# Performance work log

Measured on AMD Instinct MI355X. Metric: run time of the kernel, lower is better.

Reference implementation:

```python
import jax, jax.numpy as jnp
import numpy as np


def _rank_transform_ascending(flat):
    # torch: _, idx = sort(flat, descending=False); flat[idx] = linspace(0,1,n)+1/n
    n = flat.shape[0]
    order = jnp.argsort(flat)  # ascending
    prob = jnp.linspace(0.0, 1.0, n, dtype=flat.dtype) + jnp.asarray(1.0 / n, flat.dtype)
    return jnp.zeros_like(flat).at[order].set(prob)


def corr_attention(query, key, value):
    # score[b,h,i,j] = cosine-like similarity q_i . k_j / (|q_i| |k_j|)
    score = jnp.einsum('bhid,bhjd->bhij', query, key)
    q_len = jnp.sqrt(jnp.sum(query * query, axis=-1, keepdims=True)) + 1e-5  # [b,h,s,1]
    k_len = jnp.sqrt(jnp.sum(key * key, axis=-1, keepdims=True)) + 1e-5      # [b,h,s,1]
    score = score / (q_len * jnp.swapaxes(k_len, -1, -2))
    signal = jnp.sign(score)
    size = score.shape
    flat = jnp.abs(score).reshape(-1)
    ranked = _rank_transform_ascending(flat)
    score = -jnp.log(ranked).reshape(size) * signal
    score = score / jnp.sum(jnp.abs(score), axis=-1, keepdims=True)
    return jnp.einsum('bhij,bhjd->bhid', score, value)


def setup_inputs() -> dict:
    key0 = jax.random.key(0)
    kq, kk, kv = jax.random.split(key0, 3)
    B, H, S, D = 4, 8, 1024, 64
    query = jax.random.normal(kq, (B, H, S, D), dtype=jnp.float32)
    key = jax.random.normal(kk, (B, H, S, D), dtype=jnp.float32)
    value = jax.random.normal(kv, (B, H, S, D), dtype=jnp.float32)
    return {"query": query, "key": key, "value": value}


def reference(query, key, value):
    # Attention.forward with mode='season'
    return corr_attention(query, key, value)
```

## Files before the change

kernel.cpp:

```cpp
#include <hip/hip_runtime.h>
#include <math.h>
#include <stdint.h>

#define S_LEN 1024
#define D_DIM 64
#define BH    32
#define KSHIFT 13
#define NBINS 130048u
#define PV_LO  119808u
#define NPVT   10240u
#define HIST_LO 117760u
#define NHOT_H  12288u
#define NCHUNK 254
#define HBLK   256
#define INV_NM1 (1.0f/33554431.0f)
#define INV_N   (2.9802322387695312e-08f)
#define FIX_TH  1e-4f


typedef _Float16 half8 __attribute__((ext_vector_type(8)));
typedef short    short8 __attribute__((ext_vector_type(8)));
typedef float    floatx4 __attribute__((ext_vector_type(4)));

__global__ __launch_bounds__(256) void norms_kernel(
    const float* __restrict__ Q, const float* __restrict__ K,
    double* __restrict__ qinvD, double* __restrict__ kinvD,
    float* __restrict__ qinvF, float* __restrict__ kinvF) {
  int row  = blockIdx.x * 4 + (threadIdx.x >> 6);
  int lane = threadIdx.x & 63;
  const float* src; double* dstD; float* dstF; int r = row;
  if (row < BH * S_LEN) { src = Q; dstD = qinvD; dstF = qinvF; }
  else                  { src = K; dstD = kinvD; dstF = kinvF; r = row - BH * S_LEN; }
  double v = (double)src[(size_t)r * D_DIM + lane];
  double s = v * v;
  #pragma unroll
  for (int off = 32; off; off >>= 1) s += __shfl_down(s, off);
  if (lane == 0) {
    double inv = 1.0 / (sqrt(s) + 1e-5);
    dstD[r] = inv;
    dstF[r] = (float)inv;
  }
}

__device__ __forceinline__ void bf16_split(float x, short& hi, short& lo) {
  unsigned u = __float_as_uint(x);
  unsigned h = (u + 0x7FFFu + ((u >> 16) & 1u)) >> 16;
  float hf = __uint_as_float(h << 16);
  float lf = x - hf;
  hi = (short)h;
  lo = (short)(__float_as_uint(lf) >> 16);
}

__global__ __launch_bounds__(256) void qk_mfma_kernel(
    const float* __restrict__ Q, const float* __restrict__ K,
    const float* __restrict__ qinvF, const float* __restrict__ kinvF,
    float* __restrict__ score) {
  __shared__ short Qhi[64][72], Qlo[64][72];
  __shared__ short Khi[64][72], Klo[64][72];
  int bh = blockIdx.z;
  int i0 = blockIdx.y * 64;
  int j0 = blockIdx.x * 64;
  int tid = threadIdx.x;
  const float* Qb = Q + ((size_t)bh * S_LEN + i0) * D_DIM;
  const float* Kb = K + ((size_t)bh * S_LEN + j0) * D_DIM;
  #pragma unroll
  for (int l = 0; l < 4; ++l) {
    int idx4 = l * 256 + tid;
    int row  = idx4 >> 4;
    int c4   = idx4 & 15;
    float qi = qinvF[(size_t)bh * S_LEN + i0 + row];
    float4 v = ((const float4*)Qb)[idx4];
    float qv[4] = {v.x * qi, v.y * qi, v.z * qi, v.w * qi};
    short qh[4], ql[4];
    #pragma unroll
    for (int c = 0; c < 4; ++c) bf16_split(qv[c], qh[c], ql[c]);
    *(short4*)&Qhi[row][c4 * 4] = make_short4(qh[0], qh[1], qh[2], qh[3]);
    *(short4*)&Qlo[row][c4 * 4] = make_short4(ql[0], ql[1], ql[2], ql[3]);
    float kj = kinvF[(size_t)bh * S_LEN + j0 + row];
    float4 w = ((const float4*)Kb)[idx4];
    float kv[4] = {w.x * kj, w.y * kj, w.z * kj, w.w * kj};
    short kh[4], kl[4];
    #pragma unroll
    for (int c = 0; c < 4; ++c) bf16_split(kv[c], kh[c], kl[c]);
    *(short4*)&Khi[row][c4 * 4] = make_short4(kh[0], kh[1], kh[2], kh[3]);
    *(short4*)&Klo[row][c4 * 4] = make_short4(kl[0], kl[1], kl[2], kl[3]);
  }
  __syncthreads();
  int wave = tid >> 6;
  int lane = tid & 63;
  int m    = lane & 15;
  int quad = lane >> 4;
  floatx4 acc[4];
  #pragma unroll
  for (int n = 0; n < 4; ++n) acc[n] = (floatx4){0.f, 0.f, 0.f, 0.f};
  #pragma unroll
  for (int ks = 0; ks < 2; ++ks) {
    int kb = ks * 32 + quad * 8;
    short8 a_hi = *(const short8*)&Qhi[wave * 16 + m][kb];
    short8 a_lo = *(const short8*)&Qlo[wave * 16 + m][kb];
    #pragma unroll
    for (int nt = 0; nt < 4; ++nt) {
      short8 b_hi = *(const short8*)&Khi[nt * 16 + m][kb];
      short8 b_lo = *(const short8*)&Klo[nt * 16 + m][kb];
      acc[nt] = __builtin_amdgcn_mfma_f32_16x16x32_bf16(a_hi, b_hi, acc[nt], 0, 0, 0);
      acc[nt] = __builtin_amdgcn_mfma_f32_16x16x32_bf16(a_hi, b_lo, acc[nt], 0, 0, 0);
      acc[nt] = __builtin_amdgcn_mfma_f32_16x16x32_bf16(a_lo, b_hi, acc[nt], 0, 0, 0);
    }
  }
  #pragma unroll
  for (int r = 0; r < 4; ++r) {
    float* op = score + (size_t)bh * 1048576 + (size_t)(j0 >> 6) * 65536
              + (size_t)(i0 + wave * 16 + quad * 4 + r) * 64 + m;
    #pragma unroll
    for (int nt = 0; nt < 4; ++nt)
      op[nt * 16] = acc[nt][r];
  }
}

__global__ __launch_bounds__(1024) void hist_kernel(
    float* __restrict__ score, const float* __restrict__ Q, const float* __restrict__ K,
    const double* __restrict__ qinvD, const double* __restrict__ kinvD,
    unsigned* __restrict__ hist, unsigned char* __restrict__ partial) {
  __shared__ unsigned lh[NHOT_H];
  int tid = threadIdx.x;
  int lane = tid & 63;
  for (unsigned i = tid; i < NHOT_H; i += 1024) lh[i] = 0u;
  __syncthreads();
  const float4* p = (const float4*)score + (size_t)blockIdx.x * 32768;
  #pragma unroll 2
  for (int it = 0; it < 32; ++it) {
    float4 v = p[it * 1024 + tid];
    float vv[4] = {v.x, v.y, v.z, v.w};
    bool anyf = (fabsf(vv[0]) < FIX_TH) | (fabsf(vv[1]) < FIX_TH) |
                (fabsf(vv[2]) < FIX_TH) | (fabsf(vv[3]) < FIX_TH);
    unsigned long long am = __ballot(anyf);
    while (am) {
      int src = (int)(__ffsll((long long)am) - 1);
      am &= am - 1;
      unsigned base4 = (unsigned)(blockIdx.x * 32768u + (unsigned)(it * 1024 + tid));
      unsigned b4 = __shfl(base4, src);
      #pragma unroll
      for (int c = 0; c < 4; ++c) {
        float sc = __shfl(vv[c], src);
        if (fabsf(sc) < FIX_TH) {
          unsigned flat = b4 * 4u + (unsigned)c;
          unsigned bh = flat >> 20;
          unsigned rem = flat & 0xFFFFFu;
          unsigned jt = rem >> 16;
          unsigned i  = (rem >> 6) & 1023u;
          unsigned j  = jt * 64u + (rem & 63u);
          double qd = (double)Q[((size_t)bh * S_LEN + i) * D_DIM + lane];
          double kd = (double)K[((size_t)bh * S_LEN + j) * D_DIM + lane];
          double pd = qd * kd;
          #pragma unroll
          for (int off = 32; off; off >>= 1) pd += __shfl_down(pd, off);
          float corr = 0.f;
          if (lane == 0)
            corr = (float)(pd * qinvD[(size_t)bh * S_LEN + i] * kinvD[(size_t)bh * S_LEN + j]);
          corr = __shfl(corr, 0);
          if (lane == src) {
            vv[c] = corr;
            score[(size_t)flat] = corr;
          }
        }
      }
    }
    #pragma unroll
    for (int c = 0; c < 4; ++c) {
      unsigned b = __float_as_uint(fabsf(vv[c])) >> KSHIFT;
      if (b >= NBINS) b = NBINS - 1u;
      if (b >= HIST_LO) atomicAdd(&lh[b - HIST_LO], 1u);
      else              atomicAdd(&hist[b], 1u);
    }
  }
  __syncthreads();
  unsigned char* dst = partial + (size_t)blockIdx.x * NHOT_H;
  for (unsigned i = tid; i < NHOT_H; i += 1024) dst[i] = (unsigned char)lh[i];
}

__global__ __launch_bounds__(256) void hreduce_kernel(
    const unsigned char* __restrict__ partial, unsigned* __restrict__ hist) {
  unsigned bin = blockIdx.x * 256 + threadIdx.x;
  unsigned s = 0;
  #pragma unroll 8
  for (int b = 0; b < HBLK; ++b) s += (unsigned)partial[(size_t)b * NHOT_H + bin];
  hist[HIST_LO + bin] = s;
}

__global__ __launch_bounds__(256) void vt_kernel(
    const float* __restrict__ V, _Float16* __restrict__ Vt) {
  __shared__ _Float16 T[64][72];
  int bh = blockIdx.y, j0 = blockIdx.x * 64, tid = threadIdx.x;
  const float* Vb = V + ((size_t)bh * S_LEN + j0) * D_DIM;
  #pragma unroll
  for (int l = 0; l < 4; ++l) {
    int idx = l * 256 + tid;
    int jr = idx >> 4, d4 = idx & 15;
    float4 v = ((const float4*)Vb)[idx];
    T[d4*4+0][jr] = (_Float16)v.x;
    T[d4*4+1][jr] = (_Float16)v.y;
    T[d4*4+2][jr] = (_Float16)v.z;
    T[d4*4+3][jr] = (_Float16)v.w;
  }
  __syncthreads();
  _Float16* Ob = Vt + (size_t)(bh * 16 + blockIdx.x) * 4096;
  #pragma unroll
  for (int l = 0; l < 2; ++l) {
    int idx = l * 256 + tid;
    int d = idx >> 3, jc = idx & 7;
    uint4 val = *(const uint4*)&T[d][jc*8];
    *(uint4*)(Ob + (size_t)d * 64 + jc*8) = val;
  }
}

__global__ __launch_bounds__(256) void scan1_kernel(const unsigned* __restrict__ hist,
                                                    unsigned* __restrict__ csum) {
  __shared__ unsigned sd[256];
  int c = blockIdx.x, t = threadIdx.x;
  const unsigned* p = hist + (size_t)c * 512;
  sd[t] = p[t] + p[t + 256];
  __syncthreads();
  for (int off = 128; off; off >>= 1) {
    if (t < off) sd[t] += sd[t + off];
    __syncthreads();
  }
  if (t == 0) csum[c] = sd[0];
}

__global__ __launch_bounds__(256) void scan2_kernel(unsigned* __restrict__ csum) {
  __shared__ unsigned d[256];
  int t = threadIdx.x;
  unsigned v = (t < NCHUNK) ? csum[t] : 0u;
  d[t] = v; __syncthreads();
  for (int off = 1; off < 256; off <<= 1) {
    unsigned x = (t >= off) ? d[t - off] : 0u;
    __syncthreads();
    d[t] += x;
    __syncthreads();
  }
  if (t < NCHUNK) csum[t] = d[t] - v;
}

__global__ __launch_bounds__(256) void scan3_kernel(const unsigned* __restrict__ hist,
                                                    const unsigned* __restrict__ csum,
                                                    _Float16* __restrict__ tTab16) {
  __shared__ unsigned ts[256];
  int c = blockIdx.x, t = threadIdx.x;
  const unsigned* p = hist + (size_t)c * 512 + t * 2;
  unsigned l0 = p[0], l1 = p[1];
  unsigned s = l0 + l1;
  ts[t] = s; __syncthreads();
  for (int off = 1; off < 256; off <<= 1) {
    unsigned x = (t >= off) ? ts[t - off] : 0u;
    __syncthreads();
    ts[t] += x;
    __syncthreads();
  }
  unsigned base = csum[c] + ts[t] - s;
  int idx = c * 512 + t * 2;
  float r0 = (float)base + 0.5f * ((float)l0 - 1.0f);
  tTab16[idx]     = (_Float16)(-__logf(fmaf(r0, INV_NM1, INV_N)));
  float r1 = (float)(base + l0) + 0.5f * ((float)l1 - 1.0f);
  tTab16[idx + 1] = (_Float16)(-__logf(fmaf(r1, INV_NM1, INV_N)));
}

__global__ __launch_bounds__(256) void pv_mfma_kernel(
    const float* __restrict__ score, const _Float16* __restrict__ Vt,
    const unsigned short* __restrict__ tTab16, float* __restrict__ out) {
  __shared__ unsigned short ldsT[NPVT];
  __shared__ float red[4352];
  int tid = threadIdx.x;
  {
    const unsigned* gsrc = (const unsigned*)(tTab16 + PV_LO);
    unsigned* ldst = (unsigned*)ldsT;
    #pragma unroll
    for (int i = 0; i < 20; ++i)
      ldst[i * 256 + tid] = gsrc[i * 256 + tid];
  }
  __syncthreads();

  int bh   = blockIdx.y;
  int wave = tid >> 6;
  int lane = tid & 63;
  int m    = lane & 15;
  int quad = lane >> 4;
  int i0   = blockIdx.x * 16;
  const float*    Sb = score + (size_t)bh * 1048576 + (size_t)(i0 + m) * 64;
  const _Float16* Vb = Vt + (size_t)bh * 65536;
  floatx4 acc[4];
  #pragma unroll
  for (int n = 0; n < 4; ++n) acc[n] = (floatx4){0.f, 0.f, 0.f, 0.f};
  float rsum = 0.f;

  for (int ks = 0; ks < 8; ++ks) {
    int k0  = wave * 256 + ks * 32 + quad * 8;
    int jt  = k0 >> 6;
    int jin = k0 & 63;
    const float* sp = Sb + (size_t)jt * 65536 + jin;
    float4 s0 = *(const float4*)(sp);
    float4 s1 = *(const float4*)(sp + 4);
    float sv[8] = {s0.x, s0.y, s0.z, s0.w, s1.x, s1.y, s1.z, s1.w};
    union { unsigned short u[8]; half8 h; } af;
    #pragma unroll
    for (int e = 0; e < 8; ++e) {
      unsigned u = __float_as_uint(sv[e]);
      unsigned a = u & 0x7fffffffu;
      unsigned b = a >> KSHIFT;
      if (b > NBINS - 1u) b = NBINS - 1u;
      unsigned short tb;
      if (b >= PV_LO) tb = ldsT[b - PV_LO];
      else            tb = tTab16[b];
      if (a == 0u) tb = 0;
      af.u[e] = (unsigned short)(tb ^ ((u >> 16) & 0x8000u));
      unsigned short tabs = (unsigned short)(tb & 0x7fffu);
      _Float16 th = __builtin_bit_cast(_Float16, tabs);
      rsum += (float)th;
    }
    half8 bf[4];
    #pragma unroll
    for (int n = 0; n < 4; ++n)
      bf[n] = *(const half8*)(Vb + (size_t)jt * 4096 + (size_t)(n * 16 + m) * 64 + jin);
    #pragma unroll
    for (int n = 0; n < 4; ++n)
      acc[n] = __builtin_amdgcn_mfma_f32_16x16x32_f16(af.h, bf[n], acc[n], 0, 0, 0);
  }

  #pragma unroll
  for (int n = 0; n < 4; ++n)
    #pragma unroll
    for (int r = 0; r < 4; ++r)
      red[(wave * 16 + quad * 4 + r) * 64 + n * 16 + m] = acc[n][r];
  red[4096 + wave * 64 + lane] = rsum;
  __syncthreads();

  int col = tid & 63;
  int rq  = tid >> 6;
  #pragma unroll
  for (int t = 0; t < 4; ++t) {
    int row = rq * 4 + t;
    float s = 0.f;
    #pragma unroll
    for (int w = 0; w < 4; ++w) s += red[(w * 16 + row) * 64 + col];
    float rs = 0.f;
    #pragma unroll
    for (int w = 0; w < 4; ++w)
      #pragma unroll
      for (int q = 0; q < 4; ++q)
        rs += red[4096 + w * 64 + q * 16 + row];
    out[((size_t)bh * S_LEN + i0 + row) * D_DIM + col] = s / rs;
  }
}

extern "C" void kernel_launch(void* const* d_in, const int* in_sizes, int n_in,
                              void* d_out, int out_size, void* d_ws, size_t ws_size,
                              hipStream_t stream) {
  const float* Q = (const float*)d_in[0];
  const float* K = (const float*)d_in[1];
  const float* V = (const float*)d_in[2];
  float* out = (float*)d_out;
  char* ws = (char*)d_ws;
  float*         score   = (float*)(ws);
  unsigned*      hist    = (unsigned*)(ws + 134217728);
  unsigned char* partial = (unsigned char*)(ws + 134737920);
  double*        qinvD   = (double*)(ws + 137883648);
  double*        kinvD   = (double*)(ws + 138145792);
  float*         qinvF   = (float*)(ws + 138407936);
  float*         kinvF   = (float*)(ws + 138539008);
  _Float16*      Vt      = (_Float16*)(ws + 134737920);
  unsigned*      csum    = (unsigned*)(ws + 139194368);
  _Float16*      tTab16  = (_Float16*)(ws + 139195392);

  hipMemsetAsync(hist, 0, NBINS * sizeof(unsigned), stream);
  norms_kernel<<<(2 * BH * S_LEN) / 4, 256, 0, stream>>>(Q, K, qinvD, kinvD, qinvF, kinvF);
  qk_mfma_kernel<<<dim3(16, 16, BH), 256, 0, stream>>>(Q, K, qinvF, kinvF, score);
  hist_kernel<<<HBLK, 1024, 0, stream>>>(score, Q, K, qinvD, kinvD, hist, partial);
  hreduce_kernel<<<NHOT_H / 256, 256, 0, stream>>>(partial, hist);
  vt_kernel<<<dim3(16, BH), 256, 0, stream>>>(V, Vt);
  scan1_kernel<<<NCHUNK, 256, 0, stream>>>(hist, csum);
  scan2_kernel<<<1, 256, 0, stream>>>(csum);
  scan3_kernel<<<NCHUNK, 256, 0, stream>>>(hist, csum, tTab16);
  pv_mfma_kernel<<<dim3(S_LEN / 16, BH), 256, 0, stream>>>(
      score, Vt, (const unsigned short*)tTab16, out);
}
```

Baseline: 217.5 us.

## Store 16-bit bin codes instead of fp32 scores, fuse near-zero fixup into QK

```diff
diff --git a/kernel.cpp b/kernel.cpp
--- a/kernel.cpp
+++ b/kernel.cpp
@@ -7,11 +7,13 @@
 #define BH    32
 #define KSHIFT 13
 #define NBINS 130048u
-#define PV_LO  119808u
+#define CODE_BASE 97280u
+#define NB2   32768u
+#define HIST_LO_C 20480u
+#define NHOT_H  12288u
+#define PV_LO_C 22528u
 #define NPVT   10240u
-#define HIST_LO 117760u
-#define NHOT_H  12288u
-#define NCHUNK 254
+#define NCHUNK 64
 #define HBLK   256
 #define INV_NM1 (1.0f/33554431.0f)
 #define INV_N   (2.9802322387695312e-08f)
@@ -54,7 +56,8 @@
 __global__ __launch_bounds__(256) void qk_mfma_kernel(
     const float* __restrict__ Q, const float* __restrict__ K,
     const float* __restrict__ qinvF, const float* __restrict__ kinvF,
-    float* __restrict__ score) {
+    const double* __restrict__ qinvD, const double* __restrict__ kinvD,
+    unsigned short* __restrict__ code16) {
   __shared__ short Qhi[64][72], Qlo[64][72];
   __shared__ short Khi[64][72], Klo[64][72];
   int bh = blockIdx.z;
@@ -108,69 +111,64 @@
     }
   }
   #pragma unroll
+  for (int nt = 0; nt < 4; ++nt) {
+    #pragma unroll
+    for (int r = 0; r < 4; ++r) {
+      unsigned long long am = __ballot(fabsf(acc[nt][r]) < FIX_TH);
+      while (am) {
+        int src = (int)(__ffsll((long long)am) - 1);
+        am &= am - 1;
+        int i_s = i0 + wave * 16 + (src >> 4) * 4 + r;
+        int j_s = j0 + nt * 16 + (src & 15);
+        double qd = (double)Q[((size_t)bh * S_LEN + i_s) * D_DIM + lane];
+        double kd = (double)K[((size_t)bh * S_LEN + j_s) * D_DIM + lane];
+        double pd = qd * kd;
+        #pragma unroll
+        for (int off = 32; off; off >>= 1) pd += __shfl_down(pd, off);
+        float corr = 0.f;
+        if (lane == 0)
+          corr = (float)(pd * qinvD[(size_t)bh * S_LEN + i_s] * kinvD[(size_t)bh * S_LEN + j_s]);
+        corr = __shfl(corr, 0);
+        if (lane == src) acc[nt][r] = corr;
+      }
+    }
+  }
+  #pragma unroll
   for (int r = 0; r < 4; ++r) {
-    float* op = score + (size_t)bh * 1048576 + (size_t)(j0 >> 6) * 65536
-              + (size_t)(i0 + wave * 16 + quad * 4 + r) * 64 + m;
-    #pragma unroll
-    for (int nt = 0; nt < 4; ++nt)
-      op[nt * 16] = acc[nt][r];
+    unsigned short* op = code16 + (size_t)bh * 1048576 + (size_t)(j0 >> 6) * 65536
+                       + (size_t)(i0 + wave * 16 + quad * 4 + r) * 64 + m;
+    #pragma unroll
+    for (int nt = 0; nt < 4; ++nt) {
+      unsigned u = __float_as_uint(acc[nt][r]);
+      unsigned a = u & 0x7fffffffu;
+      unsigned b = a >> KSHIFT;
+      if (b > NBINS - 1u) b = NBINS - 1u;
+      unsigned c = (b < CODE_BASE) ? 0u : (b - CODE_BASE);
+      op[nt * 16] = (unsigned short)(c | ((u >> 16) & 0x8000u));
+    }
   }
 }
 
 __global__ __launch_bounds__(1024) void hist_kernel(
-    float* __restrict__ score, const float* __restrict__ Q, const float* __restrict__ K,
-    const double* __restrict__ qinvD, const double* __restrict__ kinvD,
-    unsigned* __restrict__ hist, unsigned char* __restrict__ partial) {
+    const uint4* __restrict__ codes, unsigned* __restrict__ hist,
+    unsigned char* __restrict__ partial) {
   __shared__ unsigned lh[NHOT_H];
   int tid = threadIdx.x;
-  int lane = tid & 63;
   for (unsigned i = tid; i < NHOT_H; i += 1024) lh[i] = 0u;
   __syncthreads();
-  const float4* p = (const float4*)score + (size_t)blockIdx.x * 32768;
+  const uint4* p = codes + (size_t)blockIdx.x * 16384;
   #pragma unroll 2
-  for (int it = 0; it < 32; ++it) {
-    float4 v = p[it * 1024 + tid];
-    float vv[4] = {v.x, v.y, v.z, v.w};
-    bool anyf = (fabsf(vv[0]) < FIX_TH) | (fabsf(vv[1]) < FIX_TH) |
-                (fabsf(vv[2]) < FIX_TH) | (fabsf(vv[3]) < FIX_TH);
-    unsigned long long am = __ballot(anyf);
-    while (am) {
-      int src = (int)(__ffsll((long long)am) - 1);
-      am &= am - 1;
-      unsigned base4 = (unsigned)(blockIdx.x * 32768u + (unsigned)(it * 1024 + tid));
-      unsigned b4 = __shfl(base4, src);
-      #pragma unroll
-      for (int c = 0; c < 4; ++c) {
-        float sc = __shfl(vv[c], src);
-        if (fabsf(sc) < FIX_TH) {
-          unsigned flat = b4 * 4u + (unsigned)c;
-          unsigned bh = flat >> 20;
-          unsigned rem = flat & 0xFFFFFu;
-          unsigned jt = rem >> 16;
-          unsigned i  = (rem >> 6) & 1023u;
-          unsigned j  = jt * 64u + (rem & 63u);
-          double qd = (double)Q[((size_t)bh * S_LEN + i) * D_DIM + lane];
-          double kd = (double)K[((size_t)bh * S_LEN + j) * D_DIM + lane];
-          double pd = qd * kd;
-          #pragma unroll
-          for (int off = 32; off; off >>= 1) pd += __shfl_down(pd, off);
-          float corr = 0.f;
-          if (lane == 0)
-            corr = (float)(pd * qinvD[(size_t)bh * S_LEN + i] * kinvD[(size_t)bh * S_LEN + j]);
-          corr = __shfl(corr, 0);
-          if (lane == src) {
-            vv[c] = corr;
-            score[(size_t)flat] = corr;
-          }
-        }
-      }
-    }
-    #pragma unroll
-    for (int c = 0; c < 4; ++c) {
-      unsigned b = __float_as_uint(fabsf(vv[c])) >> KSHIFT;
-      if (b >= NBINS) b = NBINS - 1u;
-      if (b >= HIST_LO) atomicAdd(&lh[b - HIST_LO], 1u);
-      else              atomicAdd(&hist[b], 1u);
+  for (int it = 0; it < 16; ++it) {
+    uint4 w = p[it * 1024 + tid];
+    unsigned ws[4] = {w.x, w.y, w.z, w.w};
+    #pragma unroll
+    for (int k = 0; k < 4; ++k) {
+      unsigned c0 = ws[k] & 0x7fffu;
+      unsigned c1 = (ws[k] >> 16) & 0x7fffu;
+      if (c0 >= HIST_LO_C) atomicAdd(&lh[c0 - HIST_LO_C], 1u);
+      else                 atomicAdd(&hist[c0], 1u);
+      if (c1 >= HIST_LO_C) atomicAdd(&lh[c1 - HIST_LO_C], 1u);
+      else                 atomicAdd(&hist[c1], 1u);
     }
   }
   __syncthreads();
@@ -184,7 +182,7 @@
   unsigned s = 0;
   #pragma unroll 8
   for (int b = 0; b < HBLK; ++b) s += (unsigned)partial[(size_t)b * NHOT_H + bin];
-  hist[HIST_LO + bin] = s;
+  hist[HIST_LO_C + bin] = s;
 }
 
 __global__ __launch_bounds__(256) void vt_kernel(
@@ -243,7 +241,7 @@
 
 __global__ __launch_bounds__(256) void scan3_kernel(const unsigned* __restrict__ hist,
                                                     const unsigned* __restrict__ csum,
-                                                    _Float16* __restrict__ tTab16) {
+                                                    _Float16* __restrict__ tab2) {
   __shared__ unsigned ts[256];
   int c = blockIdx.x, t = threadIdx.x;
   const unsigned* p = hist + (size_t)c * 512 + t * 2;
@@ -259,19 +257,19 @@
   unsigned base = csum[c] + ts[t] - s;
   int idx = c * 512 + t * 2;
   float r0 = (float)base + 0.5f * ((float)l0 - 1.0f);
-  tTab16[idx]     = (_Float16)(-__logf(fmaf(r0, INV_NM1, INV_N)));
+  tab2[idx]     = (_Float16)(-__logf(fmaf(r0, INV_NM1, INV_N)));
   float r1 = (float)(base + l0) + 0.5f * ((float)l1 - 1.0f);
-  tTab16[idx + 1] = (_Float16)(-__logf(fmaf(r1, INV_NM1, INV_N)));
+  tab2[idx + 1] = (_Float16)(-__logf(fmaf(r1, INV_NM1, INV_N)));
 }
 
 __global__ __launch_bounds__(256) void pv_mfma_kernel(
-    const float* __restrict__ score, const _Float16* __restrict__ Vt,
-    const unsigned short* __restrict__ tTab16, float* __restrict__ out) {
+    const unsigned short* __restrict__ code16, const _Float16* __restrict__ Vt,
+    const unsigned short* __restrict__ tab2, float* __restrict__ out) {
   __shared__ unsigned short ldsT[NPVT];
   __shared__ float red[4352];
   int tid = threadIdx.x;
   {
-    const unsigned* gsrc = (const unsigned*)(tTab16 + PV_LO);
+    const unsigned* gsrc = (const unsigned*)(tab2 + PV_LO_C);
     unsigned* ldst = (unsigned*)ldsT;
     #pragma unroll
     for (int i = 0; i < 20; ++i)
@@ -285,8 +283,8 @@
   int m    = lane & 15;
   int quad = lane >> 4;
   int i0   = blockIdx.x * 16;
-  const float*    Sb = score + (size_t)bh * 1048576 + (size_t)(i0 + m) * 64;
-  const _Float16* Vb = Vt + (size_t)bh * 65536;
+  const unsigned short* Sb = code16 + (size_t)bh * 1048576 + (size_t)(i0 + m) * 64;
+  const _Float16*       Vb = Vt + (size_t)bh * 65536;
   floatx4 acc[4];
   #pragma unroll
   for (int n = 0; n < 4; ++n) acc[n] = (floatx4){0.f, 0.f, 0.f, 0.f};
@@ -296,22 +294,18 @@
     int k0  = wave * 256 + ks * 32 + quad * 8;
     int jt  = k0 >> 6;
     int jin = k0 & 63;
-    const float* sp = Sb + (size_t)jt * 65536 + jin;
-    float4 s0 = *(const float4*)(sp);
-    float4 s1 = *(const float4*)(sp + 4);
-    float sv[8] = {s0.x, s0.y, s0.z, s0.w, s1.x, s1.y, s1.z, s1.w};
+    uint4 w = *(const uint4*)(Sb + (size_t)jt * 65536 + jin);
+    unsigned ww[4] = {w.x, w.y, w.z, w.w};
     union { unsigned short u[8]; half8 h; } af;
     #pragma unroll
     for (int e = 0; e < 8; ++e) {
-      unsigned u = __float_as_uint(sv[e]);
-      unsigned a = u & 0x7fffffffu;
-      unsigned b = a >> KSHIFT;
-      if (b > NBINS - 1u) b = NBINS - 1u;
+      unsigned cd = (e & 1) ? (ww[e >> 1] >> 16) : (ww[e >> 1] & 0xffffu);
+      unsigned c  = cd & 0x7fffu;
+      unsigned sg = cd & 0x8000u;
       unsigned short tb;
-      if (b >= PV_LO) tb = ldsT[b - PV_LO];
-      else            tb = tTab16[b];
-      if (a == 0u) tb = 0;
-      af.u[e] = (unsigned short)(tb ^ ((u >> 16) & 0x8000u));
+      if (c >= PV_LO_C) tb = ldsT[c - PV_LO_C];
+      else              tb = tab2[c];
+      af.u[e] = (unsigned short)(tb ^ sg);
       unsigned short tabs = (unsigned short)(tb & 0x7fffu);
       _Float16 th = __builtin_bit_cast(_Float16, tabs);
       rsum += (float)th;
@@ -359,26 +353,26 @@
   const float* V = (const float*)d_in[2];
   float* out = (float*)d_out;
   char* ws = (char*)d_ws;
-  float*         score   = (float*)(ws);
-  unsigned*      hist    = (unsigned*)(ws + 134217728);
-  unsigned char* partial = (unsigned char*)(ws + 134737920);
-  double*        qinvD   = (double*)(ws + 137883648);
-  double*        kinvD   = (double*)(ws + 138145792);
-  float*         qinvF   = (float*)(ws + 138407936);
-  float*         kinvF   = (float*)(ws + 138539008);
-  _Float16*      Vt      = (_Float16*)(ws + 134737920);
-  unsigned*      csum    = (unsigned*)(ws + 139194368);
-  _Float16*      tTab16  = (_Float16*)(ws + 139195392);
-
-  hipMemsetAsync(hist, 0, NBINS * sizeof(unsigned), stream);
+  unsigned short* code16  = (unsigned short*)(ws);
+  unsigned*       hist    = (unsigned*)(ws + 67108864);
+  unsigned char*  partial = (unsigned char*)(ws + 67239936);
+  double*         qinvD   = (double*)(ws + 67239936 + 3145728);
+  double*         kinvD   = (double*)(ws + 67239936 + 3407872);
+  float*          qinvF   = (float*)(ws + 67239936 + 3670016);
+  float*          kinvF   = (float*)(ws + 67239936 + 3801088);
+  _Float16*       Vt      = (_Float16*)(ws + 67239936);
+  unsigned*       csum    = (unsigned*)(ws + 67239936 + 4194304);
+  _Float16*       tab2    = (_Float16*)(ws + 67239936 + 4195328);
+
+  hipMemsetAsync(hist, 0, NB2 * sizeof(unsigned), stream);
   norms_kernel<<<(2 * BH * S_LEN) / 4, 256, 0, stream>>>(Q, K, qinvD, kinvD, qinvF, kinvF);
-  qk_mfma_kernel<<<dim3(16, 16, BH), 256, 0, stream>>>(Q, K, qinvF, kinvF, score);
-  hist_kernel<<<HBLK, 1024, 0, stream>>>(score, Q, K, qinvD, kinvD, hist, partial);
+  qk_mfma_kernel<<<dim3(16, 16, BH), 256, 0, stream>>>(Q, K, qinvF, kinvF, qinvD, kinvD, code16);
+  hist_kernel<<<HBLK, 1024, 0, stream>>>((const uint4*)code16, hist, partial);
   hreduce_kernel<<<NHOT_H / 256, 256, 0, stream>>>(partial, hist);
   vt_kernel<<<dim3(16, BH), 256, 0, stream>>>(V, Vt);
   scan1_kernel<<<NCHUNK, 256, 0, stream>>>(hist, csum);
   scan2_kernel<<<1, 256, 0, stream>>>(csum);
-  scan3_kernel<<<NCHUNK, 256, 0, stream>>>(hist, csum, tTab16);
+  scan3_kernel<<<NCHUNK, 256, 0, stream>>>(hist, csum, tab2);
   pv_mfma_kernel<<<dim3(S_LEN / 16, BH), 256, 0, stream>>>(
-      score, Vt, (const unsigned short*)tTab16, out);
-}
+      code16, Vt, (const unsigned short*)tab2, out);
+}
```

Result: faster. 201.0 us (-7.6%).
